# Kernel optimization log

Measured on AMD Instinct MI355X. Metric: run time of the kernel, lower is better.

## Reference

```python
import jax, jax.numpy as jnp
import numpy as np

DIM = 256
DIM_HEAD = 32
HEADS = DIM // DIM_HEAD
SCALE = DIM_HEAD ** -0.5


def setup_inputs() -> dict:
    key = jax.random.key(0)
    ks = jax.random.split(key, 8)
    D1 = DIM + 1
    s = 1.0 / np.sqrt(D1)
    x = jax.random.normal(ks[0], (2, 32, 32, 8, 8, D1), dtype=jnp.float32)
    Wqv = jax.random.normal(ks[1], (D1, DIM), dtype=jnp.float32) * s
    Wkv = jax.random.normal(ks[2], (D1, DIM), dtype=jnp.float32) * s
    Wvv = jax.random.normal(ks[3], (D1, DIM), dtype=jnp.float32) * s
    Wqd = jax.random.normal(ks[4], (D1, 1), dtype=jnp.float32) * s
    Wkd = jax.random.normal(ks[5], (D1, 1), dtype=jnp.float32) * s
    Wvd = jax.random.normal(ks[6], (D1, 1), dtype=jnp.float32) * s
    Wout = jax.random.normal(ks[7], (D1, D1), dtype=jnp.float32) * s
    return {"x": x, "Wqv": Wqv, "Wkv": Wkv, "Wvv": Wvv,
            "Wqd": Wqd, "Wkd": Wkd, "Wvd": Wvd, "Wout": Wout}


def reference(x, Wqv, Wkv, Wvv, Wqd, Wkd, Wvd, Wout):
    b, gx, gy, w1, w2, D1 = x.shape
    B = b * gx * gy          # number of windows
    n = w1 * w2              # tokens per window
    h, dh = HEADS, DIM_HEAD
    xf = x.reshape(B, n, D1)

    def split_heads(t, nh, d):
        # (B, n, nh*d) -> (B, nh, n, d)
        return t.reshape(B, n, nh, d).transpose(0, 2, 1, 3)

    qv = split_heads(xf @ Wqv, h, dh) * SCALE
    kv = split_heads(xf @ Wkv, h, dh)
    vv = split_heads(xf @ Wvv, h, dh)
    qd = split_heads(xf @ Wqd, 1, 1) * SCALE
    kd = split_heads(xf @ Wkd, 1, 1)
    vd = split_heads(xf @ Wvd, 1, 1)

    sim_v = jnp.einsum('bhid,bhjd->bhij', qv, kv)          # (B, h, n, n)
    sim_d = jnp.einsum('bhid,bhjd->bhij', qd, kd)          # (B, 1, n, n)
    sim_m = sim_v * jax.nn.sigmoid(sim_d)                  # depth-gated scores

    attn_v = jax.nn.softmax(sim_m, axis=-1)                # (B, h, n, n)
    attn_d = jax.nn.softmax(jnp.sum(sim_m, axis=1, keepdims=True), axis=-1)  # (B,1,n,n)

    out_v = jnp.einsum('bhij,bhjd->bhid', attn_v, vv)      # (B, h, n, dh)
    out_d = jnp.einsum('bhij,bhjd->bhid', attn_d, vd)      # (B, 1, n, 1)

    out_v = out_v.transpose(0, 2, 1, 3).reshape(B, n, h * dh)  # (B, n, dim)
    out_d = out_d.transpose(0, 2, 1, 3).reshape(B, n, 1)       # (B, n, 1)

    out = jnp.concatenate([out_v, out_d], axis=-1) @ Wout      # (B, n, dim+1)
    return out.reshape(b, gx, gy, w1, w2, D1)
```

## Files before the change

### kernel.cpp

```cpp
#include <hip/hip_runtime.h>


#define D1    257
#define NTOK  64
#define NH    8
#define KT    9
#define NT_CAT 49
#define NT_OUT 17
#define SCALE 0.17677669529663687f

#define XS_OFF    0
#define XS_STRIDE 296
#define OC_STRIDE 296
#define QS_OFF    37888
#define QK_STRIDE 264
#define AT_STRIDE 68
#define KS_OFF    72704
#define VS_OFF    106496
#define DS_OFF    139264
#define DS_STRIDE 65
#define QD_OFF    155904
#define KD_OFF    156160
#define VD_OFF    156416
#define LDS_SIZE  156672

#define WCAT_ELEMS (KT * NT_CAT * 512)
#define WOUT_ELEMS (KT * NT_OUT * 512)

using bf16x8 = __attribute__((ext_vector_type(8))) short;
using s16x4  = __attribute__((ext_vector_type(4))) short;
using f32x4  = __attribute__((ext_vector_type(4))) float;

__device__ __forceinline__ short f2b(float f) {
  unsigned u = __float_as_uint(f);
  u = (u + 0x7FFFu + ((u >> 16) & 1u)) >> 16;
  return (short)u;
}

__device__ __forceinline__ f32x4 mfma16(bf16x8 a, bf16x8 b, f32x4 c) {
  return __builtin_amdgcn_mfma_f32_16x16x32_bf16(a, b, c, 0, 0, 0);
}

__global__ void prep_weights(const float* __restrict__ Wqv, const float* __restrict__ Wkv,
                             const float* __restrict__ Wvv, const float* __restrict__ Wqd,
                             const float* __restrict__ Wkd, const float* __restrict__ Wvd,
                             const float* __restrict__ Wout,
                             short* __restrict__ wcatp, short* __restrict__ woutp) {
  int idx = blockIdx.x * 256 + threadIdx.x;
  if (idx < WCAT_ELEMS) {
    int j = idx & 7, lane = (idx >> 3) & 63, rest = idx >> 9;
    int nt = rest % NT_CAT, kt = rest / NT_CAT;
    int k = 32 * kt + (lane >> 4) * 8 + j;
    int n = 16 * nt + (lane & 15);
    float v = 0.f;
    if (k < D1) {
      if (n < 256)       v = Wqv[k * 256 + n] * SCALE;
      else if (n < 512)  v = Wkv[k * 256 + (n - 256)];
      else if (n < 768)  v = Wvv[k * 256 + (n - 512)];
      else if (n == 768) v = Wqd[k] * SCALE;
      else if (n == 769) v = Wkd[k];
      else if (n == 770) v = Wvd[k];
    }
    wcatp[idx] = f2b(v);
  } else {
    int i2 = idx - WCAT_ELEMS;
    int j = i2 & 7, lane = (i2 >> 3) & 63, rest = i2 >> 9;
    int nt = rest % NT_OUT, kt = rest / NT_OUT;
    int k = 32 * kt + (lane >> 4) * 8 + j;
    int n = 16 * nt + (lane & 15);
    float v = (k < D1 && n < D1) ? Wout[k * D1 + n] : 0.f;
    woutp[i2] = f2b(v);
  }
}

__global__ __launch_bounds__(1024)
void vda_attn(const float* __restrict__ x, const short* __restrict__ wcatp,
              const short* __restrict__ woutp, float* __restrict__ out) {
  extern __shared__ char smem[];
  short* xs  = (short*)(smem + XS_OFF);
  short* qs  = (short*)(smem + QS_OFF);
  short* ks  = (short*)(smem + KS_OFF);
  short* vs  = (short*)(smem + VS_OFF);
  float* dsum = (float*)(smem + DS_OFF);
  float* qd_s = (float*)(smem + QD_OFF);
  float* kd_s = (float*)(smem + KD_OFF);
  float* vd_s = (float*)(smem + VD_OFF);
  short* oc = xs;

  const int tid  = threadIdx.x;
  const int lane = tid & 63;
  const int w    = tid >> 6;
  const int m    = lane & 15;
  const int q    = lane >> 4;
  const int q8   = q * 8;
  const int win  = blockIdx.x;

  for (int i = tid; i < 64 * 39; i += 1024) {
    int r = i / 39, c = 257 + (i % 39);
    xs[r * XS_STRIDE + c] = 0;
  }
  for (int i = tid; i < 64 * DS_STRIDE; i += 1024) dsum[i] = 0.f;
  {
    const float4* xw4 = (const float4*)(x + (size_t)win * (NTOK * D1));
    for (int f4 = tid; f4 < 4112; f4 += 1024) {
      float4 v = xw4[f4];
      float vals[4] = {v.x, v.y, v.z, v.w};
      int o0 = f4 * 4;
      int r0 = o0 / D1, c0 = o0 - r0 * D1;
#pragma unroll
      for (int jj = 0; jj < 4; ++jj) {
        int c = c0 + jj, r = r0;
        if (c >= D1) { c -= D1; r += 1; }
        xs[r * XS_STRIDE + c] = f2b(vals[jj]);
      }
    }
  }
  __syncthreads();

  {
    f32x4 acc[4][4];
#pragma unroll
    for (int t = 0; t < 4; ++t)
#pragma unroll
      for (int mt = 0; mt < 4; ++mt) acc[t][mt] = f32x4{0.f, 0.f, 0.f, 0.f};

    for (int kt = 0; kt < KT; ++kt) {
      bf16x8 af[4];
#pragma unroll
      for (int mt = 0; mt < 4; ++mt)
        af[mt] = *(const bf16x8*)&xs[(16 * mt + m) * XS_STRIDE + 32 * kt + q8];
#pragma unroll
      for (int t = 0; t < 4; ++t) {
        int nt = w + 16 * t;
        if (nt < NT_CAT) {
          bf16x8 bfr = *(const bf16x8*)(wcatp + ((size_t)(kt * NT_CAT + nt) * 64 + lane) * 8);
#pragma unroll
          for (int mt = 0; mt < 4; ++mt)
            acc[t][mt] = mfma16(af[mt], bfr, acc[t][mt]);
        }
      }
    }
#pragma unroll
    for (int t = 0; t < 4; ++t) {
      int nt = w + 16 * t;
      if (nt >= NT_CAT) continue;
      int c = nt * 16 + m;
      if (c < 256) {
#pragma unroll
        for (int mt = 0; mt < 4; ++mt)
#pragma unroll
          for (int r = 0; r < 4; ++r)
            qs[(16 * mt + 4 * q + r) * QK_STRIDE + c] = f2b(acc[t][mt][r]);
      } else if (c < 512) {
#pragma unroll
        for (int mt = 0; mt < 4; ++mt)
#pragma unroll
          for (int r = 0; r < 4; ++r)
            ks[(16 * mt + 4 * q + r) * QK_STRIDE + (c - 256)] = f2b(acc[t][mt][r]);
      } else if (c < 768) {
#pragma unroll
        for (int mt = 0; mt < 4; ++mt) {
          int frag = (nt - 32) * 2 + (mt >> 1);
          int q2 = (2 * mt + (q >> 1)) & 3;
          int j0 = 4 * (q & 1);
          s16x4 pk;
#pragma unroll
          for (int r = 0; r < 4; ++r) pk[r] = f2b(acc[t][mt][r]);
          *(s16x4*)&vs[frag * 512 + (q2 * 16 + m) * 8 + j0] = pk;
        }
      } else {
        if (m < 3) {
          float* dst = (m == 0) ? qd_s : (m == 1) ? kd_s : vd_s;
#pragma unroll
          for (int mt = 0; mt < 4; ++mt)
#pragma unroll
            for (int r = 0; r < 4; ++r)
              dst[16 * mt + 4 * q + r] = acc[t][mt][r];
        }
      }
    }
  }
  __syncthreads();

  const int rw = w & 3;
  const int hp = w >> 2;

  bf16x8 aq[2];
#pragma unroll
  for (int hh = 0; hh < 2; ++hh)
    aq[hh] = *(const bf16x8*)&qs[(16 * rw + m) * QK_STRIDE + 32 * (2 * hp + hh) + q8];

  float gate[4][4], ssum[4][4];
  {
    float qd_r[4], kd_c[4];
#pragma unroll
    for (int r = 0; r < 4; ++r) qd_r[r] = qd_s[16 * rw + 4 * q + r];
#pragma unroll
    for (int nt = 0; nt < 4; ++nt) kd_c[nt] = kd_s[16 * nt + m];
#pragma unroll
    for (int nt = 0; nt < 4; ++nt)
#pragma unroll
      for (int r = 0; r < 4; ++r) {
        float t = qd_r[r] * kd_c[nt];
        gate[nt][r] = 1.f / (1.f + __expf(-t));
        ssum[nt][r] = 0.f;
      }
  }
  __syncthreads();

  if (hp == 0) {
    bf16x8 z = {0, 0, 0, 0, 0, 0, 0, 0};
    *(bf16x8*)&oc[(16 * rw + m) * OC_STRIDE + 256 + q8] = z;
  }

  short* atw = (short*)(smem + QS_OFF) + w * (16 * AT_STRIDE);

#pragma unroll
  for (int hh = 0; hh < 2; ++hh) {
    int h = 2 * hp + hh;
    f32x4 sv[4];
#pragma unroll
    for (int nt = 0; nt < 4; ++nt) {
      bf16x8 bk = *(const bf16x8*)&ks[(16 * nt + m) * QK_STRIDE + 32 * h + q8];
      f32x4 z = {0.f, 0.f, 0.f, 0.f};
      sv[nt] = mfma16(aq[hh], bk, z);
    }
    float sm[4][4], mx[4], sum[4];
#pragma unroll
    for (int r = 0; r < 4; ++r) mx[r] = -3.4e38f;
#pragma unroll
    for (int nt = 0; nt < 4; ++nt)
#pragma unroll
      for (int r = 0; r < 4; ++r) {
        float s = sv[nt][r] * gate[nt][r];
        ssum[nt][r] += s;
        sm[nt][r] = s;
        mx[r] = fmaxf(mx[r], s);
      }
#pragma unroll
    for (int r = 0; r < 4; ++r) {
#pragma unroll
      for (int msk = 1; msk < 16; msk <<= 1)
        mx[r] = fmaxf(mx[r], __shfl_xor(mx[r], msk));
      sum[r] = 0.f;
    }
#pragma unroll
    for (int nt = 0; nt < 4; ++nt)
#pragma unroll
      for (int r = 0; r < 4; ++r) {
        float p = __expf(sm[nt][r] - mx[r]);
        sm[nt][r] = p;
        sum[r] += p;
      }
#pragma unroll
    for (int r = 0; r < 4; ++r) {
#pragma unroll
      for (int msk = 1; msk < 16; msk <<= 1)
        sum[r] += __shfl_xor(sum[r], msk);
      sum[r] = 1.f / sum[r];
    }
#pragma unroll
    for (int nt = 0; nt < 4; ++nt)
#pragma unroll
      for (int r = 0; r < 4; ++r)
        atw[(4 * q + r) * AT_STRIDE + 16 * nt + m] = f2b(sm[nt][r] * sum[r]);

    s16x4 l0 = *(const s16x4*)&atw[m * AT_STRIDE + q8];
    s16x4 l1 = *(const s16x4*)&atw[m * AT_STRIDE + q8 + 4];
    s16x4 l2 = *(const s16x4*)&atw[m * AT_STRIDE + 32 + q8];
    s16x4 l3 = *(const s16x4*)&atw[m * AT_STRIDE + 32 + q8 + 4];
    bf16x8 a0, a1;
#pragma unroll
    for (int j = 0; j < 4; ++j) { a0[j] = l0[j]; a0[4 + j] = l1[j]; a1[j] = l2[j]; a1[4 + j] = l3[j]; }

#pragma unroll
    for (int ntp = 0; ntp < 2; ++ntp) {
      bf16x8 bv0 = *(const bf16x8*)&vs[(((2 * h + ntp) * 2) + 0) * 512 + lane * 8];
      bf16x8 bv1 = *(const bf16x8*)&vs[(((2 * h + ntp) * 2) + 1) * 512 + lane * 8];
      f32x4 o = {0.f, 0.f, 0.f, 0.f};
      o = mfma16(a0, bv0, o);
      o = mfma16(a1, bv1, o);
#pragma unroll
      for (int r = 0; r < 4; ++r)
        oc[(16 * rw + 4 * q + r) * OC_STRIDE + 32 * h + 16 * ntp + m] = f2b(o[r]);
    }
  }

#pragma unroll
  for (int nt = 0; nt < 4; ++nt)
#pragma unroll
    for (int r = 0; r < 4; ++r)
      atomicAdd(&dsum[(16 * rw + 4 * q + r) * DS_STRIDE + 16 * nt + m], ssum[nt][r]);
  __syncthreads();

  if (hp == 0) {
    float sd[4][4], mx[4], sum[4];
#pragma unroll
    for (int nt = 0; nt < 4; ++nt)
#pragma unroll
      for (int r = 0; r < 4; ++r)
        sd[nt][r] = dsum[(16 * rw + 4 * q + r) * DS_STRIDE + 16 * nt + m];
#pragma unroll
    for (int r = 0; r < 4; ++r) mx[r] = -3.4e38f;
#pragma unroll
    for (int nt = 0; nt < 4; ++nt)
#pragma unroll
      for (int r = 0; r < 4; ++r) mx[r] = fmaxf(mx[r], sd[nt][r]);
#pragma unroll
    for (int r = 0; r < 4; ++r) {
#pragma unroll
      for (int msk = 1; msk < 16; msk <<= 1)
        mx[r] = fmaxf(mx[r], __shfl_xor(mx[r], msk));
      sum[r] = 0.f;
    }
#pragma unroll
    for (int nt = 0; nt < 4; ++nt)
#pragma unroll
      for (int r = 0; r < 4; ++r) {
        sd[nt][r] = __expf(sd[nt][r] - mx[r]);
        sum[r] += sd[nt][r];
      }
#pragma unroll
    for (int r = 0; r < 4; ++r) {
#pragma unroll
      for (int msk = 1; msk < 16; msk <<= 1)
        sum[r] += __shfl_xor(sum[r], msk);
      sum[r] = 1.f / sum[r];
    }
    float vd_c[4];
#pragma unroll
    for (int nt = 0; nt < 4; ++nt) vd_c[nt] = vd_s[16 * nt + m];
    float ov[4] = {0.f, 0.f, 0.f, 0.f};
#pragma unroll
    for (int nt = 0; nt < 4; ++nt)
#pragma unroll
      for (int r = 0; r < 4; ++r) ov[r] += sd[nt][r] * vd_c[nt];
#pragma unroll
    for (int r = 0; r < 4; ++r) {
#pragma unroll
      for (int msk = 1; msk < 16; msk <<= 1)
        ov[r] += __shfl_xor(ov[r], msk);
    }
    if (m == 0) {
#pragma unroll
      for (int r = 0; r < 4; ++r)
        oc[(16 * rw + 4 * q + r) * OC_STRIDE + 256] = f2b(ov[r] * sum[r]);
    }
  }
  __syncthreads();

  {
    f32x4 acc2[2][4];
#pragma unroll
    for (int t = 0; t < 2; ++t)
#pragma unroll
      for (int mt = 0; mt < 4; ++mt) acc2[t][mt] = f32x4{0.f, 0.f, 0.f, 0.f};

    for (int kt = 0; kt < KT; ++kt) {
      bf16x8 ao[4];
#pragma unroll
      for (int mt = 0; mt < 4; ++mt)
        ao[mt] = *(const bf16x8*)&oc[(16 * mt + m) * OC_STRIDE + 32 * kt + q8];
#pragma unroll
      for (int t = 0; t < 2; ++t) {
        int nt = w + 16 * t;
        if (nt < NT_OUT) {
          bf16x8 bw = *(const bf16x8*)(woutp + ((size_t)(kt * NT_OUT + nt) * 64 + lane) * 8);
#pragma unroll
          for (int mt = 0; mt < 4; ++mt)
            acc2[t][mt] = mfma16(ao[mt], bw, acc2[t][mt]);
        }
      }
    }
#pragma unroll
    for (int t = 0; t < 2; ++t) {
      int nt = w + 16 * t;
      if (nt >= NT_OUT) continue;
      int n = 16 * nt + m;
      if (n < D1) {
#pragma unroll
        for (int mt = 0; mt < 4; ++mt)
#pragma unroll
          for (int r = 0; r < 4; ++r)
            out[((size_t)win * NTOK + 16 * mt + 4 * q + r) * D1 + n] = acc2[t][mt][r];
      }
    }
  }
}

extern "C" void kernel_launch(void* const* d_in, const int* in_sizes, int n_in,
                              void* d_out, int out_size, void* d_ws, size_t ws_size,
                              hipStream_t stream) {
  (void)n_in; (void)out_size; (void)ws_size;
  const float* x    = (const float*)d_in[0];
  const float* Wqv  = (const float*)d_in[1];
  const float* Wkv  = (const float*)d_in[2];
  const float* Wvv  = (const float*)d_in[3];
  const float* Wqd  = (const float*)d_in[4];
  const float* Wkd  = (const float*)d_in[5];
  const float* Wvd  = (const float*)d_in[6];
  const float* Wout = (const float*)d_in[7];
  float* out = (float*)d_out;

  short* wcatp = (short*)d_ws;
  short* woutp = wcatp + WCAT_ELEMS;

  int nwin = in_sizes[0] / (NTOK * D1);

  hipFuncSetAttribute((const void*)vda_attn, hipFuncAttributeMaxDynamicSharedMemorySize, LDS_SIZE);

  int prep_blocks = (WCAT_ELEMS + WOUT_ELEMS) / 256;
  prep_weights<<<prep_blocks, 256, 0, stream>>>(Wqv, Wkv, Wvv, Wqd, Wkd, Wvd, Wout, wcatp, woutp);
  vda_attn<<<nwin, 1024, LDS_SIZE, stream>>>(x, wcatp, woutp, out);
}
```

Measured before the change: 567.1 us.

## Split fused window attention into projection and attention kernels via workspace

Replaces the single fused kernel, which used 156 KB of LDS and one 1024-thread block per CU, with two kernels. The first computes the bf16 Q/K/V and depth projections into workspace. The second runs attention plus the output projection with 512 threads and about 72 KB of LDS, so several blocks can be resident per CU. The extra global round trip of the intermediates is meant to be repaid by higher occupancy. Windows are processed in chunks sized to the available workspace, and the old fused kernel remains as a fallback when the workspace is too small.

Result: slower. 818.4 us (+44.3%).

```diff
diff --git a/kernel.cpp b/kernel.cpp
--- a/kernel.cpp
+++ b/kernel.cpp
@@ -3,7 +3,6 @@
 
 #define D1    257
 #define NTOK  64
-#define NH    8
 #define KT    9
 #define NT_CAT 49
 #define NT_OUT 17
@@ -23,6 +22,11 @@
 #define KD_OFF    156160
 #define VD_OFF    156416
 #define LDS_SIZE  156672
+
+#define K2_OC_OFF 0
+#define K2_DS_OFF 37888
+#define K2_AT_OFF 54528
+#define K2_LDS    71936
 
 #define WCAT_ELEMS (KT * NT_CAT * 512)
 #define WOUT_ELEMS (KT * NT_OUT * 512)
@@ -74,6 +78,304 @@
 }
 
 __global__ __launch_bounds__(1024)
+void vda_k1(const float* __restrict__ x, const short* __restrict__ wcatp,
+            short* __restrict__ qp, short* __restrict__ kp, short* __restrict__ vp,
+            float* __restrict__ dp, int win0) {
+  __shared__ short xs[64 * XS_STRIDE];
+
+  const int tid  = threadIdx.x;
+  const int lane = tid & 63;
+  const int w    = tid >> 6;
+  const int m    = lane & 15;
+  const int q    = lane >> 4;
+  const int q8   = q * 8;
+  const int widx = blockIdx.x;
+  const int win  = win0 + widx;
+
+  for (int i = tid; i < 64 * 39; i += 1024) {
+    int r = i / 39, c = 257 + (i % 39);
+    xs[r * XS_STRIDE + c] = 0;
+  }
+  {
+    const float4* xw4 = (const float4*)(x + (size_t)win * (NTOK * D1));
+    for (int f4 = tid; f4 < 4112; f4 += 1024) {
+      float4 v = xw4[f4];
+      float vals[4] = {v.x, v.y, v.z, v.w};
+      int o0 = f4 * 4;
+      int r0 = o0 / D1, c0 = o0 - r0 * D1;
+#pragma unroll
+      for (int jj = 0; jj < 4; ++jj) {
+        int c = c0 + jj, r = r0;
+        if (c >= D1) { c -= D1; r += 1; }
+        xs[r * XS_STRIDE + c] = f2b(vals[jj]);
+      }
+    }
+  }
+  __syncthreads();
+
+  f32x4 acc[4][4];
+#pragma unroll
+  for (int t = 0; t < 4; ++t)
+#pragma unroll
+    for (int mt = 0; mt < 4; ++mt) acc[t][mt] = f32x4{0.f, 0.f, 0.f, 0.f};
+
+  for (int kt = 0; kt < KT; ++kt) {
+    bf16x8 af[4];
+#pragma unroll
+    for (int mt = 0; mt < 4; ++mt)
+      af[mt] = *(const bf16x8*)&xs[(16 * mt + m) * XS_STRIDE + 32 * kt + q8];
+#pragma unroll
+    for (int t = 0; t < 4; ++t) {
+      int nt = w + 16 * t;
+      if (nt < NT_CAT) {
+        bf16x8 bfr = *(const bf16x8*)(wcatp + ((size_t)(kt * NT_CAT + nt) * 64 + lane) * 8);
+#pragma unroll
+        for (int mt = 0; mt < 4; ++mt)
+          acc[t][mt] = mfma16(af[mt], bfr, acc[t][mt]);
+      }
+    }
+  }
+
+  short* qpw = qp + (size_t)widx * 16384;
+  short* kpw = kp + (size_t)widx * 16384;
+  short* vpw = vp + (size_t)widx * 16384;
+  float* dpw = dp + (size_t)widx * 192;
+#pragma unroll
+  for (int t = 0; t < 4; ++t) {
+    int nt = w + 16 * t;
+    if (nt >= NT_CAT) continue;
+    int c = nt * 16 + m;
+    if (c < 256) {
+#pragma unroll
+      for (int mt = 0; mt < 4; ++mt)
+#pragma unroll
+        for (int r = 0; r < 4; ++r)
+          qpw[(16 * mt + 4 * q + r) * 256 + c] = f2b(acc[t][mt][r]);
+    } else if (c < 512) {
+      int cc = c - 256;
+#pragma unroll
+      for (int mt = 0; mt < 4; ++mt)
+#pragma unroll
+        for (int r = 0; r < 4; ++r)
+          kpw[(16 * mt + 4 * q + r) * 256 + cc] = f2b(acc[t][mt][r]);
+    } else if (c < 768) {
+#pragma unroll
+      for (int mt = 0; mt < 4; ++mt) {
+        int frag = (nt - 32) * 2 + (mt >> 1);
+        int q2 = (2 * mt + (q >> 1)) & 3;
+        int j0 = 4 * (q & 1);
+        s16x4 pk;
+#pragma unroll
+        for (int r = 0; r < 4; ++r) pk[r] = f2b(acc[t][mt][r]);
+        *(s16x4*)&vpw[frag * 512 + (q2 * 16 + m) * 8 + j0] = pk;
+      }
+    } else if (m < 3) {
+      float* dst = dpw + m * 64;
+#pragma unroll
+      for (int mt = 0; mt < 4; ++mt)
+#pragma unroll
+        for (int r = 0; r < 4; ++r)
+          dst[16 * mt + 4 * q + r] = acc[t][mt][r];
+    }
+  }
+}
+
+__global__ __launch_bounds__(512, 4)
+void vda_k2(const short* __restrict__ qp, const short* __restrict__ kp,
+            const short* __restrict__ vp, const float* __restrict__ dp,
+            const short* __restrict__ woutp, float* __restrict__ out, int win0) {
+  extern __shared__ char smem[];
+  short* oc   = (short*)(smem + K2_OC_OFF);
+  float* dsum = (float*)(smem + K2_DS_OFF);
+  short* atb  = (short*)(smem + K2_AT_OFF);
+
+  const int tid  = threadIdx.x;
+  const int lane = tid & 63;
+  const int h    = tid >> 6;
+  const int m    = lane & 15;
+  const int q    = lane >> 4;
+  const int q8   = q * 8;
+  const int widx = blockIdx.x;
+  const int win  = win0 + widx;
+
+  for (int i = tid; i < 64 * DS_STRIDE; i += 512) dsum[i] = 0.f;
+  {
+    int r = tid >> 3, c0 = 256 + (tid & 7) * 4;
+    s16x4 z = {0, 0, 0, 0};
+    *(s16x4*)&oc[r * OC_STRIDE + c0] = z;
+  }
+  __syncthreads();
+
+  const short* qpw = qp + (size_t)widx * 16384 + 32 * h + q8;
+  const short* kpw = kp + (size_t)widx * 16384 + 32 * h + q8;
+  const short* vw  = vp + (size_t)widx * 16384 + (size_t)(4 * h) * 512 + lane * 8;
+  const float* dpw = dp + (size_t)widx * 192;
+
+  bf16x8 bk[4];
+#pragma unroll
+  for (int nt = 0; nt < 4; ++nt) bk[nt] = *(const bf16x8*)&kpw[(16 * nt + m) * 256];
+  float kd_c[4];
+#pragma unroll
+  for (int nt = 0; nt < 4; ++nt) kd_c[nt] = dpw[64 + 16 * nt + m];
+
+  short* atw = atb + h * (16 * AT_STRIDE);
+
+#pragma unroll
+  for (int mh = 0; mh < 2; ++mh) {
+    bf16x8 aq0 = *(const bf16x8*)&qpw[(16 * (2 * mh + 0) + m) * 256];
+    bf16x8 aq1 = *(const bf16x8*)&qpw[(16 * (2 * mh + 1) + m) * 256];
+    f32x4 sv[2][4];
+#pragma unroll
+    for (int nt = 0; nt < 4; ++nt) {
+      f32x4 z = {0.f, 0.f, 0.f, 0.f};
+      sv[0][nt] = mfma16(aq0, bk[nt], z);
+      sv[1][nt] = mfma16(aq1, bk[nt], z);
+    }
+#pragma unroll
+    for (int mt2 = 0; mt2 < 2; ++mt2) {
+      const int mt = 2 * mh + mt2;
+      float qd_r[4];
+#pragma unroll
+      for (int r = 0; r < 4; ++r) qd_r[r] = dpw[16 * mt + 4 * q + r];
+
+      float sm[4][4], mx[4], sum[4];
+#pragma unroll
+      for (int r = 0; r < 4; ++r) mx[r] = -3.4e38f;
+#pragma unroll
+      for (int nt = 0; nt < 4; ++nt)
+#pragma unroll
+        for (int r = 0; r < 4; ++r) {
+          float tg = qd_r[r] * kd_c[nt];
+          float g = 1.f / (1.f + __expf(-tg));
+          float s = sv[mt2][nt][r] * g;
+          sm[nt][r] = s;
+          mx[r] = fmaxf(mx[r], s);
+        }
+#pragma unroll
+      for (int nt = 0; nt < 4; ++nt)
+#pragma unroll
+        for (int r = 0; r < 4; ++r)
+          atomicAdd(&dsum[(16 * mt + 4 * q + r) * DS_STRIDE + 16 * nt + m], sm[nt][r]);
+#pragma unroll
+      for (int r = 0; r < 4; ++r) {
+#pragma unroll
+        for (int msk = 1; msk < 16; msk <<= 1)
+          mx[r] = fmaxf(mx[r], __shfl_xor(mx[r], msk));
+        sum[r] = 0.f;
+      }
+#pragma unroll
+      for (int nt = 0; nt < 4; ++nt)
+#pragma unroll
+        for (int r = 0; r < 4; ++r) {
+          float p = __expf(sm[nt][r] - mx[r]);
+          sm[nt][r] = p;
+          sum[r] += p;
+        }
+#pragma unroll
+      for (int r = 0; r < 4; ++r) {
+#pragma unroll
+        for (int msk = 1; msk < 16; msk <<= 1)
+          sum[r] += __shfl_xor(sum[r], msk);
+        sum[r] = 1.f / sum[r];
+      }
+#pragma unroll
+      for (int nt = 0; nt < 4; ++nt)
+#pragma unroll
+        for (int r = 0; r < 4; ++r)
+          atw[(4 * q + r) * AT_STRIDE + 16 * nt + m] = f2b(sm[nt][r] * sum[r]);
+
+      s16x4 l0 = *(const s16x4*)&atw[m * AT_STRIDE + q8];
+      s16x4 l1 = *(const s16x4*)&atw[m * AT_STRIDE + q8 + 4];
+      s16x4 l2 = *(const s16x4*)&atw[m * AT_STRIDE + 32 + q8];
+      s16x4 l3 = *(const s16x4*)&atw[m * AT_STRIDE + 32 + q8 + 4];
+      bf16x8 a0, a1;
+#pragma unroll
+      for (int j = 0; j < 4; ++j) { a0[j] = l0[j]; a0[4 + j] = l1[j]; a1[j] = l2[j]; a1[4 + j] = l3[j]; }
+
+#pragma unroll
+      for (int ntv = 0; ntv < 2; ++ntv) {
+        bf16x8 bv0 = *(const bf16x8*)&vw[(2 * ntv + 0) * 512];
+        bf16x8 bv1 = *(const bf16x8*)&vw[(2 * ntv + 1) * 512];
+        f32x4 o = {0.f, 0.f, 0.f, 0.f};
+        o = mfma16(a0, bv0, o);
+        o = mfma16(a1, bv1, o);
+#pragma unroll
+        for (int r = 0; r < 4; ++r)
+          oc[(16 * mt + 4 * q + r) * OC_STRIDE + 32 * h + 16 * ntv + m] = f2b(o[r]);
+      }
+    }
+  }
+  __syncthreads();
+
+  {
+    int row = 8 * h + (lane >> 3);
+    int c0 = (lane & 7) * 8;
+    float sd[8], vd[8];
+#pragma unroll
+    for (int j = 0; j < 8; ++j) sd[j] = dsum[row * DS_STRIDE + c0 + j];
+#pragma unroll
+    for (int j = 0; j < 8; ++j) vd[j] = dpw[128 + c0 + j];
+    float mx = sd[0];
+#pragma unroll
+    for (int j = 1; j < 8; ++j) mx = fmaxf(mx, sd[j]);
+#pragma unroll
+    for (int msk = 1; msk < 8; msk <<= 1) mx = fmaxf(mx, __shfl_xor(mx, msk));
+    float sum = 0.f, ov = 0.f;
+#pragma unroll
+    for (int j = 0; j < 8; ++j) {
+      float e = __expf(sd[j] - mx);
+      sum += e;
+      ov += e * vd[j];
+    }
+#pragma unroll
+    for (int msk = 1; msk < 8; msk <<= 1) { sum += __shfl_xor(sum, msk); ov += __shfl_xor(ov, msk); }
+    if ((lane & 7) == 0) oc[row * OC_STRIDE + 256] = f2b(ov / sum);
+  }
+  __syncthreads();
+
+  {
+    f32x4 acc2[5][2];
+#pragma unroll
+    for (int s = 0; s < 5; ++s) {
+      acc2[s][0] = f32x4{0.f, 0.f, 0.f, 0.f};
+      acc2[s][1] = f32x4{0.f, 0.f, 0.f, 0.f};
+    }
+    for (int kt = 0; kt < KT; ++kt) {
+      bf16x8 ao[4];
+#pragma unroll
+      for (int mt = 0; mt < 4; ++mt)
+        ao[mt] = *(const bf16x8*)&oc[(16 * mt + m) * OC_STRIDE + 32 * kt + q8];
+#pragma unroll
+      for (int s = 0; s < 5; ++s) {
+        int idx = h + 8 * s;
+        if (idx < 34) {
+          int nt = idx >> 1, mhh = idx & 1;
+          bf16x8 bw = *(const bf16x8*)(woutp + ((size_t)(kt * NT_OUT + nt) * 64 + lane) * 8);
+          acc2[s][0] = mfma16(ao[2 * mhh + 0], bw, acc2[s][0]);
+          acc2[s][1] = mfma16(ao[2 * mhh + 1], bw, acc2[s][1]);
+        }
+      }
+    }
+#pragma unroll
+    for (int s = 0; s < 5; ++s) {
+      int idx = h + 8 * s;
+      if (idx >= 34) continue;
+      int nt = idx >> 1, mhh = idx & 1;
+      int n = 16 * nt + m;
+      if (n < D1) {
+#pragma unroll
+        for (int p = 0; p < 2; ++p) {
+          int mt = 2 * mhh + p;
+#pragma unroll
+          for (int r = 0; r < 4; ++r)
+            out[((size_t)win * NTOK + 16 * mt + 4 * q + r) * D1 + n] = acc2[s][p][r];
+        }
+      }
+    }
+  }
+}
+
+__global__ __launch_bounds__(1024)
 void vda_attn(const float* __restrict__ x, const short* __restrict__ wcatp,
               const short* __restrict__ woutp, float* __restrict__ out) {
   extern __shared__ char smem[];
@@ -221,9 +523,9 @@
     f32x4 sv[4];
 #pragma unroll
     for (int nt = 0; nt < 4; ++nt) {
-      bf16x8 bk = *(const bf16x8*)&ks[(16 * nt + m) * QK_STRIDE + 32 * h + q8];
+      bf16x8 bkf = *(const bf16x8*)&ks[(16 * nt + m) * QK_STRIDE + 32 * h + q8];
       f32x4 z = {0.f, 0.f, 0.f, 0.f};
-      sv[nt] = mfma16(aq[hh], bk, z);
+      sv[nt] = mfma16(aq[hh], bkf, z);
     }
     float sm[4][4], mx[4], sum[4];
 #pragma unroll
@@ -391,7 +693,7 @@
 extern "C" void kernel_launch(void* const* d_in, const int* in_sizes, int n_in,
                               void* d_out, int out_size, void* d_ws, size_t ws_size,
                               hipStream_t stream) {
-  (void)n_in; (void)out_size; (void)ws_size;
+  (void)n_in; (void)out_size;
   const float* x    = (const float*)d_in[0];
   const float* Wqv  = (const float*)d_in[1];
   const float* Wkv  = (const float*)d_in[2];
@@ -407,9 +709,33 @@
 
   int nwin = in_sizes[0] / (NTOK * D1);
 
-  hipFuncSetAttribute((const void*)vda_attn, hipFuncAttributeMaxDynamicSharedMemorySize, LDS_SIZE);
-
   int prep_blocks = (WCAT_ELEMS + WOUT_ELEMS) / 256;
   prep_weights<<<prep_blocks, 256, 0, stream>>>(Wqv, Wkv, Wvv, Wqd, Wkd, Wvd, Wout, wcatp, woutp);
-  vda_attn<<<nwin, 1024, LDS_SIZE, stream>>>(x, wcatp, woutp, out);
+
+  const size_t woff = (size_t)(WCAT_ELEMS + WOUT_ELEMS) * 2;
+  const size_t per_win = 99072;
+  size_t avail = (ws_size > woff) ? ws_size - woff : 0;
+  long long cwll = (long long)(avail / per_win);
+  int cw = (cwll > nwin) ? nwin : (int)cwll;
+
+  if (cw < 64) {
+    hipFuncSetAttribute((const void*)vda_attn, hipFuncAttributeMaxDynamicSharedMemorySize, LDS_SIZE);
+    vda_attn<<<nwin, 1024, LDS_SIZE, stream>>>(x, wcatp, woutp, out);
+    return;
+  }
+
+  hipFuncSetAttribute((const void*)vda_k2, hipFuncAttributeMaxDynamicSharedMemorySize, K2_LDS);
+
+  char* pbase = (char*)d_ws + woff;
+  short* qp = (short*)pbase;
+  short* kp = qp + (size_t)cw * 16384;
+  short* vp = kp + (size_t)cw * 16384;
+  float* dpf = (float*)(vp + (size_t)cw * 16384);
+
+  for (int base = 0; base < nwin; base += cw) {
+    int g = nwin - base;
+    if (g > cw) g = cw;
+    vda_k1<<<g, 1024, 0, stream>>>(x, wcatp, qp, kp, vp, dpf, base);
+    vda_k2<<<g, 512, K2_LDS, stream>>>(qp, kp, vp, dpf, woutp, out, base);
+  }
 }
```

## Store LDS operands in MFMA fragment layout and software-pipeline weight loads

Applied to the files above, without the earlier changes.

Activations, Q, K and the concatenated attention output are now kept in shared memory in a pre-swizzled MFMA fragment layout, so each lane reads one contiguous 16-byte chunk instead of strided rows. The QKV projection is split into two passes with fixed per-wave tile assignments (Q/K first, then V plus the depth columns). The K loops are fully unrolled with a two-stage register prefetch of global weight fragments and one-ahead prefetch of LDS A fragments. The aim is to cut LDS bank conflicts and hide global load latency, at the cost of more registers, a second pass over the activations, and idle waves on the single extra column tile.

Measured after the change: 550.4 us. 2.9% less time.

```diff
diff --git a/kernel.cpp b/kernel.cpp
--- a/kernel.cpp
+++ b/kernel.cpp
@@ -3,26 +3,22 @@
 
 #define D1    257
 #define NTOK  64
-#define NH    8
 #define KT    9
 #define NT_CAT 49
 #define NT_OUT 17
 #define SCALE 0.17677669529663687f
 
-#define XS_OFF    0
-#define XS_STRIDE 296
-#define OC_STRIDE 296
-#define QS_OFF    37888
-#define QK_STRIDE 264
+#define XS2_OFF 0
+#define QS2_OFF 36864
+#define KS2_OFF 71680
+#define VS2_OFF 104448
+#define DS2_OFF 137216
+#define QD2_OFF 153856
+#define KD2_OFF 154112
+#define VD2_OFF 154368
+#define LDS2    154624
 #define AT_STRIDE 68
-#define KS_OFF    72704
-#define VS_OFF    106496
-#define DS_OFF    139264
 #define DS_STRIDE 65
-#define QD_OFF    155904
-#define KD_OFF    156160
-#define VD_OFF    156416
-#define LDS_SIZE  156672
 
 #define WCAT_ELEMS (KT * NT_CAT * 512)
 #define WOUT_ELEMS (KT * NT_OUT * 512)
@@ -40,6 +36,9 @@
 __device__ __forceinline__ f32x4 mfma16(bf16x8 a, bf16x8 b, f32x4 c) {
   return __builtin_amdgcn_mfma_f32_16x16x32_bf16(a, b, c, 0, 0, 0);
 }
+
+#define WFRAG(kt, nt) (*(const bf16x8*)(wcatp + ((size_t)((kt) * NT_CAT + (nt)) * 64 + lane) * 8))
+#define OFRAG(kt, nt) (*(const bf16x8*)(woutp + ((size_t)((kt) * NT_OUT + (nt)) * 64 + lane) * 8))
 
 __global__ void prep_weights(const float* __restrict__ Wqv, const float* __restrict__ Wkv,
                              const float* __restrict__ Wvv, const float* __restrict__ Wqd,
@@ -74,17 +73,17 @@
 }
 
 __global__ __launch_bounds__(1024)
-void vda_attn(const float* __restrict__ x, const short* __restrict__ wcatp,
-              const short* __restrict__ woutp, float* __restrict__ out) {
+void vda_attn2(const float* __restrict__ x, const short* __restrict__ wcatp,
+               const short* __restrict__ woutp, float* __restrict__ out) {
   extern __shared__ char smem[];
-  short* xs  = (short*)(smem + XS_OFF);
-  short* qs  = (short*)(smem + QS_OFF);
-  short* ks  = (short*)(smem + KS_OFF);
-  short* vs  = (short*)(smem + VS_OFF);
-  float* dsum = (float*)(smem + DS_OFF);
-  float* qd_s = (float*)(smem + QD_OFF);
-  float* kd_s = (float*)(smem + KD_OFF);
-  float* vd_s = (float*)(smem + VD_OFF);
+  short* xs   = (short*)(smem + XS2_OFF);
+  short* qs   = (short*)(smem + QS2_OFF);
+  short* ks   = (short*)(smem + KS2_OFF);
+  short* vs   = (short*)(smem + VS2_OFF);
+  float* dsum = (float*)(smem + DS2_OFF);
+  float* qd_s = (float*)(smem + QD2_OFF);
+  float* kd_s = (float*)(smem + KD2_OFF);
+  float* vd_s = (float*)(smem + VD2_OFF);
   short* oc = xs;
 
   const int tid  = threadIdx.x;
@@ -95,11 +94,17 @@
   const int q8   = q * 8;
   const int win  = blockIdx.x;
 
-  for (int i = tid; i < 64 * 39; i += 1024) {
-    int r = i / 39, c = 257 + (i % 39);
-    xs[r * XS_STRIDE + c] = 0;
+  bf16x8 bA0 = WFRAG(0, w),      bA1 = WFRAG(1, w);
+  bf16x8 bB0 = WFRAG(0, w + 16), bB1 = WFRAG(1, w + 16);
+
+  {
+    int4 z4; z4.x = 0; z4.y = 0; z4.z = 0; z4.w = 0;
+    int4* xz = (int4*)xs;
+    for (int i = tid; i < 2304; i += 1024) xz[i] = z4;
   }
   for (int i = tid; i < 64 * DS_STRIDE; i += 1024) dsum[i] = 0.f;
+  __syncthreads();
+
   {
     const float4* xw4 = (const float4*)(x + (size_t)win * (NTOK * D1));
     for (int f4 = tid; f4 < 4112; f4 += 1024) {
@@ -111,73 +116,121 @@
       for (int jj = 0; jj < 4; ++jj) {
         int c = c0 + jj, r = r0;
         if (c >= D1) { c -= D1; r += 1; }
-        xs[r * XS_STRIDE + c] = f2b(vals[jj]);
+        int idx = ((c >> 5) * 4 + (r >> 4)) * 512 + (((c >> 3) & 3) * 16 + (r & 15)) * 8 + (c & 7);
+        xs[idx] = f2b(vals[jj]);
       }
     }
   }
   __syncthreads();
 
   {
-    f32x4 acc[4][4];
-#pragma unroll
-    for (int t = 0; t < 4; ++t)
+    f32x4 acc[2][4];
+#pragma unroll
+    for (int t = 0; t < 2; ++t)
 #pragma unroll
       for (int mt = 0; mt < 4; ++mt) acc[t][mt] = f32x4{0.f, 0.f, 0.f, 0.f};
 
+    bf16x8 a_c[4];
+#pragma unroll
+    for (int mt = 0; mt < 4; ++mt)
+      a_c[mt] = *(const bf16x8*)&xs[mt * 512 + lane * 8];
+
+#pragma unroll
     for (int kt = 0; kt < KT; ++kt) {
-      bf16x8 af[4];
+      bf16x8 bA2{}, bB2{};
+      if (kt + 2 < KT) {
+        bA2 = WFRAG(kt + 2, w);
+        bB2 = WFRAG(kt + 2, w + 16);
+      }
+      bf16x8 a_n[4];
+      if (kt + 1 < KT) {
+#pragma unroll
+        for (int mt = 0; mt < 4; ++mt)
+          a_n[mt] = *(const bf16x8*)&xs[((kt + 1) * 4 + mt) * 512 + lane * 8];
+      }
+#pragma unroll
+      for (int mt = 0; mt < 4; ++mt) acc[0][mt] = mfma16(a_c[mt], bA0, acc[0][mt]);
+#pragma unroll
+      for (int mt = 0; mt < 4; ++mt) acc[1][mt] = mfma16(a_c[mt], bB0, acc[1][mt]);
+      bA0 = bA1; bA1 = bA2; bB0 = bB1; bB1 = bB2;
+      if (kt + 1 < KT) {
+#pragma unroll
+        for (int mt = 0; mt < 4; ++mt) a_c[mt] = a_n[mt];
+      }
+    }
+
+    bf16x8 cA0 = WFRAG(0, w + 32), cA1 = WFRAG(1, w + 32);
+    bf16x8 cB0{}, cB1{};
+    if (w == 0) { cB0 = WFRAG(0, 48); cB1 = WFRAG(1, 48); }
+
+    {
+      int cq = (2 * w + (m >> 3)) & 3;
+      int jj = m & 7;
+      int fb = (w >> 1) * 4;
 #pragma unroll
       for (int mt = 0; mt < 4; ++mt)
-        af[mt] = *(const bf16x8*)&xs[(16 * mt + m) * XS_STRIDE + 32 * kt + q8];
-#pragma unroll
-      for (int t = 0; t < 4; ++t) {
-        int nt = w + 16 * t;
-        if (nt < NT_CAT) {
-          bf16x8 bfr = *(const bf16x8*)(wcatp + ((size_t)(kt * NT_CAT + nt) * 64 + lane) * 8);
-#pragma unroll
-          for (int mt = 0; mt < 4; ++mt)
-            acc[t][mt] = mfma16(af[mt], bfr, acc[t][mt]);
-        }
-      }
-    }
-#pragma unroll
-    for (int t = 0; t < 4; ++t) {
-      int nt = w + 16 * t;
-      if (nt >= NT_CAT) continue;
-      int c = nt * 16 + m;
-      if (c < 256) {
+#pragma unroll
+        for (int r = 0; r < 4; ++r)
+          qs[(fb + mt) * 512 + (cq * 16 + 4 * q + r) * 8 + jj] = f2b(acc[0][mt][r]);
+#pragma unroll
+      for (int mt = 0; mt < 4; ++mt)
+#pragma unroll
+        for (int r = 0; r < 4; ++r)
+          ks[(fb + mt) * 512 + (cq * 16 + 4 * q + r) * 8 + jj] = f2b(acc[1][mt][r]);
+    }
+
+#pragma unroll
+    for (int t = 0; t < 2; ++t)
+#pragma unroll
+      for (int mt = 0; mt < 4; ++mt) acc[t][mt] = f32x4{0.f, 0.f, 0.f, 0.f};
+
+#pragma unroll
+    for (int mt = 0; mt < 4; ++mt)
+      a_c[mt] = *(const bf16x8*)&xs[mt * 512 + lane * 8];
+
+#pragma unroll
+    for (int kt = 0; kt < KT; ++kt) {
+      bf16x8 cA2{}, cB2{};
+      if (kt + 2 < KT) {
+        cA2 = WFRAG(kt + 2, w + 32);
+        if (w == 0) cB2 = WFRAG(kt + 2, 48);
+      }
+      bf16x8 a_n[4];
+      if (kt + 1 < KT) {
 #pragma unroll
         for (int mt = 0; mt < 4; ++mt)
-#pragma unroll
-          for (int r = 0; r < 4; ++r)
-            qs[(16 * mt + 4 * q + r) * QK_STRIDE + c] = f2b(acc[t][mt][r]);
-      } else if (c < 512) {
-#pragma unroll
-        for (int mt = 0; mt < 4; ++mt)
-#pragma unroll
-          for (int r = 0; r < 4; ++r)
-            ks[(16 * mt + 4 * q + r) * QK_STRIDE + (c - 256)] = f2b(acc[t][mt][r]);
-      } else if (c < 768) {
-#pragma unroll
-        for (int mt = 0; mt < 4; ++mt) {
-          int frag = (nt - 32) * 2 + (mt >> 1);
-          int q2 = (2 * mt + (q >> 1)) & 3;
-          int j0 = 4 * (q & 1);
-          s16x4 pk;
-#pragma unroll
-          for (int r = 0; r < 4; ++r) pk[r] = f2b(acc[t][mt][r]);
-          *(s16x4*)&vs[frag * 512 + (q2 * 16 + m) * 8 + j0] = pk;
-        }
-      } else {
-        if (m < 3) {
-          float* dst = (m == 0) ? qd_s : (m == 1) ? kd_s : vd_s;
-#pragma unroll
-          for (int mt = 0; mt < 4; ++mt)
-#pragma unroll
-            for (int r = 0; r < 4; ++r)
-              dst[16 * mt + 4 * q + r] = acc[t][mt][r];
-        }
-      }
+          a_n[mt] = *(const bf16x8*)&xs[((kt + 1) * 4 + mt) * 512 + lane * 8];
+      }
+#pragma unroll
+      for (int mt = 0; mt < 4; ++mt) acc[0][mt] = mfma16(a_c[mt], cA0, acc[0][mt]);
+      if (w == 0) {
+#pragma unroll
+        for (int mt = 0; mt < 4; ++mt) acc[1][mt] = mfma16(a_c[mt], cB0, acc[1][mt]);
+      }
+      cA0 = cA1; cA1 = cA2; cB0 = cB1; cB1 = cB2;
+      if (kt + 1 < KT) {
+#pragma unroll
+        for (int mt = 0; mt < 4; ++mt) a_c[mt] = a_n[mt];
+      }
+    }
+
+#pragma unroll
+    for (int mt = 0; mt < 4; ++mt) {
+      int frag = w * 2 + (mt >> 1);
+      int q2 = (2 * mt + (q >> 1)) & 3;
+      int j0 = 4 * (q & 1);
+      s16x4 pk;
+#pragma unroll
+      for (int r = 0; r < 4; ++r) pk[r] = f2b(acc[0][mt][r]);
+      *(s16x4*)&vs[frag * 512 + (q2 * 16 + m) * 8 + j0] = pk;
+    }
+    if (w == 0 && m < 3) {
+      float* dst = (m == 0) ? qd_s : (m == 1) ? kd_s : vd_s;
+#pragma unroll
+      for (int mt = 0; mt < 4; ++mt)
+#pragma unroll
+        for (int r = 0; r < 4; ++r)
+          dst[16 * mt + 4 * q + r] = acc[1][mt][r];
     }
   }
   __syncthreads();
@@ -188,7 +241,7 @@
   bf16x8 aq[2];
 #pragma unroll
   for (int hh = 0; hh < 2; ++hh)
-    aq[hh] = *(const bf16x8*)&qs[(16 * rw + m) * QK_STRIDE + 32 * (2 * hp + hh) + q8];
+    aq[hh] = *(const bf16x8*)&qs[(((2 * hp + hh) * 4 + rw)) * 512 + lane * 8];
 
   float gate[4][4], ssum[4][4];
   {
@@ -209,11 +262,11 @@
   __syncthreads();
 
   if (hp == 0) {
-    bf16x8 z = {0, 0, 0, 0, 0, 0, 0, 0};
-    *(bf16x8*)&oc[(16 * rw + m) * OC_STRIDE + 256 + q8] = z;
-  }
-
-  short* atw = (short*)(smem + QS_OFF) + w * (16 * AT_STRIDE);
+    int4 z4; z4.x = 0; z4.y = 0; z4.z = 0; z4.w = 0;
+    ((int4*)(oc + 32 * 512))[rw * 64 + lane] = z4;
+  }
+
+  short* atw = (short*)(smem + QS2_OFF) + w * (16 * AT_STRIDE);
 
 #pragma unroll
   for (int hh = 0; hh < 2; ++hh) {
@@ -221,7 +274,7 @@
     f32x4 sv[4];
 #pragma unroll
     for (int nt = 0; nt < 4; ++nt) {
-      bf16x8 bk = *(const bf16x8*)&ks[(16 * nt + m) * QK_STRIDE + 32 * h + q8];
+      bf16x8 bk = *(const bf16x8*)&ks[(h * 4 + nt) * 512 + lane * 8];
       f32x4 z = {0.f, 0.f, 0.f, 0.f};
       sv[nt] = mfma16(aq[hh], bk, z);
     }
@@ -274,15 +327,16 @@
     for (int j = 0; j < 4; ++j) { a0[j] = l0[j]; a0[4 + j] = l1[j]; a1[j] = l2[j]; a1[4 + j] = l3[j]; }
 
 #pragma unroll
-    for (int ntp = 0; ntp < 2; ++ntp) {
-      bf16x8 bv0 = *(const bf16x8*)&vs[(((2 * h + ntp) * 2) + 0) * 512 + lane * 8];
-      bf16x8 bv1 = *(const bf16x8*)&vs[(((2 * h + ntp) * 2) + 1) * 512 + lane * 8];
+    for (int ntv = 0; ntv < 2; ++ntv) {
+      bf16x8 bv0 = *(const bf16x8*)&vs[(((2 * h + ntv) * 2) + 0) * 512 + lane * 8];
+      bf16x8 bv1 = *(const bf16x8*)&vs[(((2 * h + ntv) * 2) + 1) * 512 + lane * 8];
       f32x4 o = {0.f, 0.f, 0.f, 0.f};
       o = mfma16(a0, bv0, o);
       o = mfma16(a1, bv1, o);
+      int cq2 = (2 * ntv + (m >> 3)) & 3;
 #pragma unroll
       for (int r = 0; r < 4; ++r)
-        oc[(16 * rw + 4 * q + r) * OC_STRIDE + 32 * h + 16 * ntp + m] = f2b(o[r]);
+        oc[(h * 4 + rw) * 512 + (cq2 * 16 + 4 * q + r) * 8 + (m & 7)] = f2b(o[r]);
     }
   }
 
@@ -344,9 +398,13 @@
     if (m == 0) {
 #pragma unroll
       for (int r = 0; r < 4; ++r)
-        oc[(16 * rw + 4 * q + r) * OC_STRIDE + 256] = f2b(ov[r] * sum[r]);
-    }
-  }
+        oc[(32 + rw) * 512 + (4 * q + r) * 8] = f2b(ov[r] * sum[r]);
+    }
+  }
+
+  bf16x8 dA0 = OFRAG(0, w), dA1 = OFRAG(1, w);
+  bf16x8 dB0{}, dB1{};
+  if (w == 0) { dB0 = OFRAG(0, 16); dB1 = OFRAG(1, 16); }
   __syncthreads();
 
   {
@@ -356,34 +414,51 @@
 #pragma unroll
       for (int mt = 0; mt < 4; ++mt) acc2[t][mt] = f32x4{0.f, 0.f, 0.f, 0.f};
 
+    bf16x8 ao_c[4];
+#pragma unroll
+    for (int mt = 0; mt < 4; ++mt)
+      ao_c[mt] = *(const bf16x8*)&oc[mt * 512 + lane * 8];
+
+#pragma unroll
     for (int kt = 0; kt < KT; ++kt) {
-      bf16x8 ao[4];
+      bf16x8 dA2{}, dB2{};
+      if (kt + 2 < KT) {
+        dA2 = OFRAG(kt + 2, w);
+        if (w == 0) dB2 = OFRAG(kt + 2, 16);
+      }
+      bf16x8 ao_n[4];
+      if (kt + 1 < KT) {
+#pragma unroll
+        for (int mt = 0; mt < 4; ++mt)
+          ao_n[mt] = *(const bf16x8*)&oc[((kt + 1) * 4 + mt) * 512 + lane * 8];
+      }
+#pragma unroll
+      for (int mt = 0; mt < 4; ++mt) acc2[0][mt] = mfma16(ao_c[mt], dA0, acc2[0][mt]);
+      if (w == 0) {
+#pragma unroll
+        for (int mt = 0; mt < 4; ++mt) acc2[1][mt] = mfma16(ao_c[mt], dB0, acc2[1][mt]);
+      }
+      dA0 = dA1; dA1 = dA2; dB0 = dB1; dB1 = dB2;
+      if (kt + 1 < KT) {
+#pragma unroll
+        for (int mt = 0; mt < 4; ++mt) ao_c[mt] = ao_n[mt];
+      }
+    }
+
+    {
+      int n = 16 * w + m;
 #pragma unroll
       for (int mt = 0; mt < 4; ++mt)
-        ao[mt] = *(const bf16x8*)&oc[(16 * mt + m) * OC_STRIDE + 32 * kt + q8];
-#pragma unroll
-      for (int t = 0; t < 2; ++t) {
-        int nt = w + 16 * t;
-        if (nt < NT_OUT) {
-          bf16x8 bw = *(const bf16x8*)(woutp + ((size_t)(kt * NT_OUT + nt) * 64 + lane) * 8);
-#pragma unroll
-          for (int mt = 0; mt < 4; ++mt)
-            acc2[t][mt] = mfma16(ao[mt], bw, acc2[t][mt]);
-        }
-      }
-    }
-#pragma unroll
-    for (int t = 0; t < 2; ++t) {
-      int nt = w + 16 * t;
-      if (nt >= NT_OUT) continue;
-      int n = 16 * nt + m;
-      if (n < D1) {
-#pragma unroll
-        for (int mt = 0; mt < 4; ++mt)
-#pragma unroll
-          for (int r = 0; r < 4; ++r)
-            out[((size_t)win * NTOK + 16 * mt + 4 * q + r) * D1 + n] = acc2[t][mt][r];
-      }
+#pragma unroll
+        for (int r = 0; r < 4; ++r)
+          out[((size_t)win * NTOK + 16 * mt + 4 * q + r) * D1 + n] = acc2[0][mt][r];
+    }
+    if (w == 0 && m == 0) {
+#pragma unroll
+      for (int mt = 0; mt < 4; ++mt)
+#pragma unroll
+        for (int r = 0; r < 4; ++r)
+          out[((size_t)win * NTOK + 16 * mt + 4 * q + r) * D1 + 256] = acc2[1][mt][r];
     }
   }
 }
@@ -407,9 +482,9 @@
 
   int nwin = in_sizes[0] / (NTOK * D1);
 
-  hipFuncSetAttribute((const void*)vda_attn, hipFuncAttributeMaxDynamicSharedMemorySize, LDS_SIZE);
-
   int prep_blocks = (WCAT_ELEMS + WOUT_ELEMS) / 256;
   prep_weights<<<prep_blocks, 256, 0, stream>>>(Wqv, Wkv, Wvv, Wqd, Wkd, Wvd, Wout, wcatp, woutp);
-  vda_attn<<<nwin, 1024, LDS_SIZE, stream>>>(x, wcatp, woutp, out);
+
+  hipFuncSetAttribute((const void*)vda_attn2, hipFuncAttributeMaxDynamicSharedMemorySize, LDS2);
+  vda_attn2<<<nwin, 1024, LDS2, stream>>>(x, wcatp, woutp, out);
 }
```
